# Performance work log

Hardware: AMD Instinct MI355X
Metric: run time of the kernel (lower is better)

Reference implementation:

```python
import jax, jax.numpy as jnp
import numpy as np

B, S, DIN, DOUT = 8, 2048, 4096, 11008


def setup_inputs() -> dict:
    key = jax.random.key(0)
    k1, k2, k3 = jax.random.split(key, 3)
    x = jax.random.normal(k1, (B, S, DIN), dtype=jnp.float32)
    # int8 quantized weight in [-128, 127]
    weight_int8 = jax.random.randint(k2, (DOUT, DIN), -128, 128, dtype=jnp.int8)
    # positive per-output-row scales
    weight_scale = jax.random.uniform(k3, (DOUT,), dtype=jnp.float32, minval=1e-4, maxval=1e-2)
    return {"x": x, "weight_int8": weight_int8, "weight_scale": weight_scale}


def reference(x, weight_int8, weight_scale):
    # dequantize: [DOUT, DIN] fp32 weight
    w_fp = weight_int8.astype(jnp.float32) * weight_scale[:, None]
    # F.linear: x @ w.T  -> [B, S, DOUT]
    return jnp.einsum('bsd,od->bso', x, w_fp)
```

## Files before the change

### kernel.cpp

```cpp
#include <hip/hip_runtime.h>
#include <cstdint>
#include <cstddef>

typedef __attribute__((ext_vector_type(4))) int int32x4;
typedef __attribute__((ext_vector_type(16))) int int32x16;

#define DEVI __device__ __forceinline__

constexpr int M = 16384;
constexpr int N = 11008;
constexpr int K = 4096;
constexpr int BM = 256, BN = 256, BK = 64;
constexpr int NT_M = M / BM;
constexpr int NT_N = N / BN;
constexpr int NTILES = K / BK;
constexpr int NWG = NT_M * NT_N;
constexpr int TILE_BYTES = BM * BK;

DEVI void gload_lds16(const void* gsrc, void* ldst) {
  __builtin_amdgcn_global_load_lds(
      (const __attribute__((address_space(1))) unsigned int*)gsrc,
      (__attribute__((address_space(3))) unsigned int*)ldst,
      16, 0, 0);
}

__global__ __launch_bounds__(256) void pack_w_kernel(const int* __restrict__ w32,
                                                     signed char* __restrict__ w8) {
  const int idx = blockIdx.x * 256 + threadIdx.x;
  const int total4 = N * K / 4;
  if (idx < total4) {
    const int4 v = ((const int4*)w32)[idx];
    ((int*)w8)[idx] = (v.x & 255) | ((v.y & 255) << 8) |
                      ((v.z & 255) << 16) | ((v.w & 255) << 24);
  }
}

__global__ __launch_bounds__(256) void quant_x_kernel(const float* __restrict__ x,
                                                      signed char* __restrict__ xq,
                                                      float* __restrict__ sx) {
  const int row = blockIdx.x;
  const int t = threadIdx.x;
  const float4* xr = (const float4*)(x + (size_t)row * K);
  float4 v[4];
  float amax = 0.f;
  #pragma unroll
  for (int c = 0; c < 4; ++c) {
    v[c] = xr[c * 256 + t];
    amax = fmaxf(amax, fmaxf(fmaxf(fabsf(v[c].x), fabsf(v[c].y)),
                             fmaxf(fabsf(v[c].z), fabsf(v[c].w))));
  }
  __shared__ float red[256];
  red[t] = amax;
  __syncthreads();
  #pragma unroll
  for (int s = 128; s >= 1; s >>= 1) {
    if (t < s) red[t] = fmaxf(red[t], red[t + s]);
    __syncthreads();
  }
  const float am = fmaxf(red[0], 1e-20f);
  const float inv = 127.f / am;
  if (t == 0) sx[row] = am * (1.f / 127.f);
  int* xq32 = (int*)(xq + (size_t)row * K);
  #pragma unroll
  for (int c = 0; c < 4; ++c) {
    int q0 = min(127, max(-127, __float2int_rn(v[c].x * inv)));
    int q1 = min(127, max(-127, __float2int_rn(v[c].y * inv)));
    int q2 = min(127, max(-127, __float2int_rn(v[c].z * inv)));
    int q3 = min(127, max(-127, __float2int_rn(v[c].w * inv)));
    xq32[c * 256 + t] = (q0 & 255) | ((q1 & 255) << 8) |
                        ((q2 & 255) << 16) | ((q3 & 255) << 24);
  }
}

__global__ __launch_bounds__(512, 2) void gemm_i8_kernel(const signed char* __restrict__ aq,
                                                         const signed char* __restrict__ wq,
                                                         const float* __restrict__ sx,
                                                         const float* __restrict__ sw,
                                                         float* __restrict__ out) {
  extern __shared__ signed char smem[];
  signed char* lsA = smem;
  signed char* lsB = smem + 4 * TILE_BYTES;

  const int tid = threadIdx.x;
  const int w = tid >> 6;
  const int l = tid & 63;

  const int bid = blockIdx.x;
  const int wg = (bid & 7) * (NWG / 8) + (bid >> 3);
  const int mt = wg / NT_N;
  const int nt = wg % NT_N;
  const int m0 = mt * BM, n0 = nt * BN;

  const bool stA = (w < 4);
  const signed char* src[4];
  int loff[4];
  #pragma unroll
  for (int c = 0; c < 4; ++c) {
    const int q = (w & 3) * 4 + c;
    const int row = (q & 3) * 64 + l;
    const int s = q >> 2;
    const signed char* base = stA ? (aq + (size_t)(m0 + row) * K)
                                  : (wq + (size_t)(n0 + row) * K);
    src[c] = base + s * 16;
    loff[c] = q * 1024;
  }

  auto STAGE = [&](int tile) {
    signed char* lbase = (stA ? lsA : lsB) + (tile & 3) * TILE_BYTES;
    const int koff = tile * BK;
    #pragma unroll
    for (int c = 0; c < 4; ++c)
      gload_lds16(src[c] + koff, lbase + loff[c]);
  };

  const int wm = w >> 2, wn = w & 3;
  const int aBase = (l >> 5) * 4096 + (wm * 128 + (l & 31)) * 16;
  const int bBase = (l >> 5) * 4096 + (wn * 64 + (l & 31)) * 16;

  int32x16 acc[4][2] = {};

  auto COMPUTE = [&](int tile) {
    const signed char* pA = lsA + (tile & 3) * TILE_BYTES;
    const signed char* pB = lsB + (tile & 3) * TILE_BYTES;
    int32x4 af[2][4], bf[2][2];
    #pragma unroll
    for (int ks = 0; ks < 2; ++ks) {
      #pragma unroll
      for (int j = 0; j < 2; ++j)
        bf[ks][j] = *(const int32x4*)(pB + bBase + ks * 8192 + j * 512);
      #pragma unroll
      for (int i = 0; i < 4; ++i)
        af[ks][i] = *(const int32x4*)(pA + aBase + ks * 8192 + i * 512);
    }
    __builtin_amdgcn_s_setprio(1);
    #pragma unroll
    for (int ks = 0; ks < 2; ++ks) {
      #pragma unroll
      for (int i = 0; i < 4; ++i) {
        #pragma unroll
        for (int j = 0; j < 2; ++j) {
          acc[i][j] = __builtin_amdgcn_mfma_i32_32x32x32_i8(af[ks][i], bf[ks][j],
                                                            acc[i][j], 0, 0, 0);
        }
      }
    }
    __builtin_amdgcn_s_setprio(0);
  };

  STAGE(0); STAGE(1); STAGE(2);
  for (int t = 0; t <= NTILES - 4; ++t) {
    asm volatile("s_waitcnt vmcnt(8)\n\ts_barrier" ::: "memory");
    STAGE(t + 3);
    COMPUTE(t);
  }
  asm volatile("s_waitcnt vmcnt(8)\n\ts_barrier" ::: "memory");
  COMPUTE(NTILES - 3);
  asm volatile("s_waitcnt vmcnt(4)\n\ts_barrier" ::: "memory");
  COMPUTE(NTILES - 2);
  asm volatile("s_waitcnt vmcnt(0)\n\ts_barrier" ::: "memory");
  COMPUTE(NTILES - 1);

  const int col = l & 31;
  const int rbase = (l >> 5) * 4;
  float swv[2];
  #pragma unroll
  for (int fj = 0; fj < 2; ++fj) swv[fj] = sw[n0 + wn * 64 + fj * 32 + col];
  #pragma unroll
  for (int fi = 0; fi < 4; ++fi) {
    #pragma unroll
    for (int r = 0; r < 16; ++r) {
      const int row = (r & 3) + 8 * (r >> 2) + rbase;
      const int grow = m0 + wm * 128 + fi * 32 + row;
      const float sxv = sx[grow];
      float* orow = out + (size_t)grow * N + n0 + wn * 64 + col;
      #pragma unroll
      for (int fj = 0; fj < 2; ++fj) {
        orow[fj * 32] = (float)acc[fi][fj][r] * sxv * swv[fj];
      }
    }
  }
}

extern "C" void kernel_launch(void* const* d_in, const int* in_sizes, int n_in,
                              void* d_out, int out_size, void* d_ws, size_t ws_size,
                              hipStream_t stream) {
  const float* x = (const float*)d_in[0];
  const int* w32 = (const int*)d_in[1];
  const float* wscale = (const float*)d_in[2];
  float* out = (float*)d_out;

  signed char* xq = (signed char*)d_ws;
  signed char* wq = xq + (size_t)M * K;
  float* sx = (float*)(wq + (size_t)N * K);

  pack_w_kernel<<<(N * K / 4 + 255) / 256, 256, 0, stream>>>(w32, wq);
  quant_x_kernel<<<M, 256, 0, stream>>>(x, xq, sx);
  gemm_i8_kernel<<<NWG, 512, 131072, stream>>>(xq, wq, sx, wscale, out);
}
```

Before: 1.050 ms.

## Split each K-tile into two half-steps with interleaved LDS reads and staging

```diff
diff --git a/kernel.cpp b/kernel.cpp
--- a/kernel.cpp
+++ b/kernel.cpp
@@ -105,60 +105,89 @@
     loff[c] = q * 1024;
   }
 
-  auto STAGE = [&](int tile) {
-    signed char* lbase = (stA ? lsA : lsB) + (tile & 3) * TILE_BYTES;
-    const int koff = tile * BK;
-    #pragma unroll
-    for (int c = 0; c < 4; ++c)
-      gload_lds16(src[c] + koff, lbase + loff[c]);
-  };
+#define STAGE_HALF(tile, h)                                                   \
+  {                                                                           \
+    signed char* lbase = (stA ? lsA : lsB) + ((tile) & 3) * TILE_BYTES;       \
+    const int koff = (tile) * BK;                                             \
+    gload_lds16(src[2 * (h)] + koff, lbase + loff[2 * (h)]);                  \
+    gload_lds16(src[2 * (h) + 1] + koff, lbase + loff[2 * (h) + 1]);          \
+  }
+
+#define STAGE_FULL(tile) STAGE_HALF(tile, 0) STAGE_HALF(tile, 1)
 
   const int wm = w >> 2, wn = w & 3;
   const int aBase = (l >> 5) * 4096 + (wm * 128 + (l & 31)) * 16;
   const int bBase = (l >> 5) * 4096 + (wn * 64 + (l & 31)) * 16;
 
   int32x16 acc[4][2] = {};
-
-  auto COMPUTE = [&](int tile) {
-    const signed char* pA = lsA + (tile & 3) * TILE_BYTES;
-    const signed char* pB = lsB + (tile & 3) * TILE_BYTES;
-    int32x4 af[2][4], bf[2][2];
-    #pragma unroll
-    for (int ks = 0; ks < 2; ++ks) {
-      #pragma unroll
-      for (int j = 0; j < 2; ++j)
-        bf[ks][j] = *(const int32x4*)(pB + bBase + ks * 8192 + j * 512);
-      #pragma unroll
-      for (int i = 0; i < 4; ++i)
-        af[ks][i] = *(const int32x4*)(pA + aBase + ks * 8192 + i * 512);
-    }
-    __builtin_amdgcn_s_setprio(1);
-    #pragma unroll
-    for (int ks = 0; ks < 2; ++ks) {
-      #pragma unroll
-      for (int i = 0; i < 4; ++i) {
-        #pragma unroll
-        for (int j = 0; j < 2; ++j) {
-          acc[i][j] = __builtin_amdgcn_mfma_i32_32x32x32_i8(af[ks][i], bf[ks][j],
-                                                            acc[i][j], 0, 0, 0);
-        }
-      }
-    }
-    __builtin_amdgcn_s_setprio(0);
-  };
-
-  STAGE(0); STAGE(1); STAGE(2);
-  for (int t = 0; t <= NTILES - 4; ++t) {
-    asm volatile("s_waitcnt vmcnt(8)\n\ts_barrier" ::: "memory");
-    STAGE(t + 3);
-    COMPUTE(t);
-  }
-  asm volatile("s_waitcnt vmcnt(8)\n\ts_barrier" ::: "memory");
-  COMPUTE(NTILES - 3);
-  asm volatile("s_waitcnt vmcnt(4)\n\ts_barrier" ::: "memory");
-  COMPUTE(NTILES - 2);
-  asm volatile("s_waitcnt vmcnt(0)\n\ts_barrier" ::: "memory");
-  COMPUTE(NTILES - 1);
+  int32x4 af[4], bf[2];
+
+#define DS_LOADS(tile, ks)                                                    \
+  {                                                                           \
+    const signed char* pA = lsA + ((tile) & 3) * TILE_BYTES;                  \
+    const signed char* pB = lsB + ((tile) & 3) * TILE_BYTES;                  \
+    const int ko = (ks) * 8192;                                               \
+    bf[0] = *(const int32x4*)(pB + bBase + ko);                               \
+    bf[1] = *(const int32x4*)(pB + bBase + ko + 512);                         \
+    af[0] = *(const int32x4*)(pA + aBase + ko);                               \
+    af[1] = *(const int32x4*)(pA + aBase + ko + 512);                         \
+    af[2] = *(const int32x4*)(pA + aBase + ko + 1024);                        \
+    af[3] = *(const int32x4*)(pA + aBase + ko + 1536);                        \
+  }
+
+#define LGKM0()                                          \
+  asm volatile("s_waitcnt lgkmcnt(0)" ::: "memory");     \
+  __builtin_amdgcn_sched_barrier(0);
+
+#define MFMA8()                                                               \
+  __builtin_amdgcn_s_setprio(1);                                              \
+  {                                                                           \
+    _Pragma("unroll")                                                         \
+    for (int i = 0; i < 4; ++i) {                                             \
+      acc[i][0] = __builtin_amdgcn_mfma_i32_32x32x32_i8(af[i], bf[0],         \
+                                                        acc[i][0], 0, 0, 0);  \
+      acc[i][1] = __builtin_amdgcn_mfma_i32_32x32x32_i8(af[i], bf[1],         \
+                                                        acc[i][1], 0, 0, 0);  \
+    }                                                                         \
+  }                                                                           \
+  __builtin_amdgcn_s_setprio(0);
+
+#define BAR() __builtin_amdgcn_s_barrier();
+
+  STAGE_FULL(0) STAGE_FULL(1) STAGE_FULL(2)
+  asm volatile("s_waitcnt vmcnt(8)" ::: "memory");
+  BAR()
+
+  #pragma unroll 4
+  for (int t = 0; t < 60; ++t) {
+    DS_LOADS(t, 0)
+    STAGE_HALF(t + 3, 0)
+    BAR()
+    LGKM0()
+    MFMA8()
+    BAR()
+    DS_LOADS(t, 1)
+    STAGE_HALF(t + 3, 1)
+    asm volatile("s_waitcnt vmcnt(8)" ::: "memory");
+    BAR()
+    LGKM0()
+    MFMA8()
+    BAR()
+  }
+  DS_LOADS(60, 0) STAGE_HALF(63, 0) BAR() LGKM0() MFMA8() BAR()
+  DS_LOADS(60, 1) STAGE_HALF(63, 1)
+  asm volatile("s_waitcnt vmcnt(8)" ::: "memory");
+  BAR() LGKM0() MFMA8() BAR()
+  DS_LOADS(61, 0) BAR() LGKM0() MFMA8() BAR()
+  DS_LOADS(61, 1)
+  asm volatile("s_waitcnt vmcnt(4)" ::: "memory");
+  BAR() LGKM0() MFMA8() BAR()
+  DS_LOADS(62, 0) BAR() LGKM0() MFMA8() BAR()
+  DS_LOADS(62, 1)
+  asm volatile("s_waitcnt vmcnt(0)" ::: "memory");
+  BAR() LGKM0() MFMA8() BAR()
+  DS_LOADS(63, 0) BAR() LGKM0() MFMA8() BAR()
+  DS_LOADS(63, 1) BAR() LGKM0() MFMA8()
 
   const int col = l & 31;
   const int rbase = (l >> 5) * 4;
```

After: 1.047 ms. No clear change (-0.3%).
